# Optimization experiments

Measured on AMD Instinct MI355X. Metric: run time of the kernel, lower is better.

Reference implementation:

```python
import jax, jax.numpy as jnp
import numpy as np

D, H, O, NEXP, NA = 128, 256, 128, 8, 5  # na = max(1, int(8*0.7)) = 5
T = float(np.e)  # gate temperature
N_TOKENS = 131072


def ternary_quantize(w):
    # per-expert-matrix threshold: alpha = mean(|W|) over each [out,in] matrix
    alpha = jnp.mean(jnp.abs(w), axis=(-2, -1), keepdims=True)
    return jnp.sign(w) * (jnp.abs(w) > 0.5 * alpha).astype(w.dtype)


def setup_inputs() -> dict:
    key = jax.random.key(0)
    ks = jax.random.split(key, 7)
    x = jax.random.normal(ks[0], (N_TOKENS, D), dtype=jnp.float32)
    # expert params stacked over expert dim e (nn.Linear layout: [out, in])
    w1 = jax.random.normal(ks[1], (NEXP, H, D), dtype=jnp.float32) * 0.05
    b1 = jax.random.normal(ks[2], (NEXP, H), dtype=jnp.float32) * 0.05
    w2 = jax.random.normal(ks[3], (NEXP, O, H), dtype=jnp.float32) * 0.05
    b2 = jax.random.normal(ks[4], (NEXP, O), dtype=jnp.float32) * 0.05
    wg = jax.random.normal(ks[5], (NEXP, D), dtype=jnp.float32) * 0.05
    bg = jax.random.normal(ks[6], (NEXP,), dtype=jnp.float32) * 0.05
    return {"x": x, "w1": w1, "b1": b1, "w2": w2, "b2": b2, "wg": wg, "bg": bg}


def reference(x, w1, b1, w2, b2, wg, bg):
    # Ternary-quantize expert weights on the fly (TW.forward); dropout in eval mode (identity).
    w1q = ternary_quantize(w1)
    w2q = ternary_quantize(w2)
    # all-expert dense MLP: x [t,d] -> hidden [t,e,h] -> eo [t,e,o]
    hid = jax.nn.relu(jnp.einsum('td,ehd->teh', x, w1q) + b1[None, :, :])
    eo = jnp.einsum('teh,eoh->teo', hid, w2q) + b2[None, :, :]
    # BG gate: tempered softmax, top-k mask, renormalize
    p = jax.nn.softmax((x @ wg.T + bg) / T, axis=-1)          # [t,e]
    _, idx = jax.lax.top_k(p, NA)                             # [t,na]
    m = jnp.sum(jax.nn.one_hot(idx, NEXP, dtype=p.dtype), axis=-2)  # [t,e] 0/1 mask
    w = p * m
    w = w / (jnp.sum(w, axis=-1, keepdims=True) + 1e-8)
    return jnp.einsum('te,teo->to', w, eo)
```

## Files before the change

kernel.cpp:

```cpp
#include <hip/hip_runtime.h>
#include <hip/hip_bf16.h>

typedef unsigned int u32;
typedef unsigned short u16;
using f32x4  = __attribute__((ext_vector_type(4))) float;
using f32x16 = __attribute__((ext_vector_type(16))) float;
using u32x4  = __attribute__((ext_vector_type(4))) u32;
using s16x8  = __attribute__((ext_vector_type(8))) short;

#define DEV static __device__ __forceinline__

DEV u32 pk2(float a, float b) {
  u16 lo = __builtin_bit_cast(u16, __float2bfloat16(a));
  u16 hi = __builtin_bit_cast(u16, __float2bfloat16(b));
  return (u32)lo | ((u32)hi << 16);
}

DEV f32x16 MFMA32(u32x4 a, u32x4 b, f32x16 c) {
  return __builtin_amdgcn_mfma_f32_32x32x16_bf16(
      __builtin_bit_cast(s16x8, a), __builtin_bit_cast(s16x8, b), c, 0, 0, 0);
}

DEV void pl32swap(u32& a, u32& b) {
  asm volatile("v_permlane32_swap_b32 %0, %1" : "+v"(a), "+v"(b));
}

typedef const __attribute__((address_space(1))) u32 gu32;
typedef __attribute__((address_space(3))) u32 lu32;

DEV void load_lds16(const void* g, void* l) {
  __builtin_amdgcn_global_load_lds((gu32*)g, (lu32*)l, 16, 0, 0);
}

__global__ void qalpha(const float* __restrict__ w1, const float* __restrict__ w2,
                       float* __restrict__ alphas) {
  int b = blockIdx.x;
  const float* src = (b < 8 ? w1 : w2) + (size_t)(b & 7) * 32768;
  int tid = threadIdx.x;
  float s = 0.f;
  for (int i = tid; i < 32768; i += 256) s += fabsf(src[i]);
  #pragma unroll
  for (int off = 32; off >= 1; off >>= 1) s += __shfl_down(s, off, 64);
  __shared__ float ws4[4];
  if ((tid & 63) == 0) ws4[tid >> 6] = s;
  __syncthreads();
  if (tid == 0) alphas[b] = (ws4[0] + ws4[1] + ws4[2] + ws4[3]) * (1.f / 32768.f);
}

DEV u16 tq1(float v, float thr) {
  return (fabsf(v) > thr) ? (v > 0.f ? (u16)0x3F80 : (u16)0xBF80) : (u16)0;
}
DEV u32 tq2(float a, float b, float thr) {
  return (u32)tq1(a, thr) | ((u32)tq1(b, thr) << 16);
}

__global__ void qimg(const float* __restrict__ w1, const float* __restrict__ w2,
                     const float* __restrict__ alphas, char* __restrict__ img) {
  int gid = blockIdx.x * 256 + threadIdx.x;
  int l = gid & 63;
  int col = l & 31, hi = l >> 5;
  const float* src;
  float thr;
  char* dst;
  if (gid < 32768) {
    int ks = (gid >> 6) & 7;
    int n  = gid >> 9;
    int e  = n >> 3, ht = n & 7;
    int h  = ht * 32 + col;
    int k0 = ks * 16 + hi * 8;
    src = w1 + (size_t)e * 32768 + h * 128 + k0;
    thr = 0.5f * alphas[e];
    dst = img + (size_t)n * 16384 + ks * 1024 + l * 16;
  } else {
    int id = gid - 32768;
    int sl = (id >> 6) & 7;
    int n  = id >> 9;
    int e  = n >> 3, c = n & 7;
    int ks2 = sl >> 2, ot = sl & 3;
    int o  = ot * 32 + col;
    int k0 = c * 32 + ks2 * 16 + hi * 8;
    src = w2 + (size_t)e * 32768 + o * 256 + k0;
    thr = 0.5f * alphas[8 + e];
    dst = img + (size_t)n * 16384 + 8192 + sl * 1024 + l * 16;
  }
  float4 v0 = *(const float4*)src;
  float4 v1 = *(const float4*)(src + 4);
  u32 q0 = tq2(v0.x, v0.y, thr), q1 = tq2(v0.z, v0.w, thr);
  u32 q2 = tq2(v1.x, v1.y, thr), q3 = tq2(v1.z, v1.w, thr);
  *(uint4*)dst = make_uint4(q0, q1, q2, q3);
}

#define B1_OFF 65536
#define G_OFF  73728
#define SMEM_BYTES 81920

__global__ __launch_bounds__(256, 2) void moe_main(
    const float* __restrict__ x, const float* __restrict__ b1g,
    const float* __restrict__ b2g, const float* __restrict__ wg,
    const float* __restrict__ bg, const char* __restrict__ img,
    float* __restrict__ out) {
  extern __shared__ char smem[];
  float* s_b1 = (float*)(smem + B1_OFF);
  float* s_g  = (float*)(smem + G_OFF);
  const int tid = threadIdx.x;
  const int w = tid >> 6, l = tid & 63;
  const int col = l & 31, hi = l >> 5;
  const int tokw = blockIdx.x * 256 + w * 64;
  const u32 loff = (u32)(l * 16);

  auto stage_pair = [&](int p) {
    const char* src = img + (size_t)p * 32768 + w * 8192 + loff;
    char* dst = smem + (p & 1) * 32768 + w * 8192;
    #pragma unroll
    for (int i = 0; i < 8; ++i)
      load_lds16(src + i * 1024, dst + i * 1024);
  };

  stage_pair(0);

  {
    const float4* s = (const float4*)b1g;
    float4* d = (float4*)s_b1;
    d[tid] = s[tid];
    d[tid + 256] = s[tid + 256];
  }

  u32x4 xf[2][8];
  #pragma unroll
  for (int tt = 0; tt < 2; ++tt) {
    #pragma unroll
    for (int ks = 0; ks < 8; ++ks) {
      const float* xp = x + (size_t)(tokw + tt * 32 + col) * 128 + ks * 16 + hi * 8;
      float4 v0 = *(const float4*)xp;
      float4 v1 = *(const float4*)(xp + 4);
      xf[tt][ks] = (u32x4){pk2(v0.x, v0.y), pk2(v0.z, v0.w),
                           pk2(v1.x, v1.y), pk2(v1.z, v1.w)};
    }
  }

  {
    int t = blockIdx.x * 256 + tid;
    const float4* xr = (const float4*)(x + (size_t)t * 128);
    const float4* wr = (const float4*)wg;
    float lg[8];
    #pragma unroll
    for (int e = 0; e < 8; ++e) lg[e] = bg[e];
    for (int i = 0; i < 32; ++i) {
      float4 xv = xr[i];
      #pragma unroll
      for (int e = 0; e < 8; ++e) {
        float4 wv = wr[e * 32 + i];
        lg[e] += xv.x * wv.x + xv.y * wv.y + xv.z * wv.z + xv.w * wv.w;
      }
    }
    const float invT = 0.36787944117144233f;
    #pragma unroll
    for (int e = 0; e < 8; ++e) lg[e] *= invT;
    float mx = lg[0];
    #pragma unroll
    for (int e = 1; e < 8; ++e) mx = fmaxf(mx, lg[e]);
    float p[8], den = 0.f;
    #pragma unroll
    for (int e = 0; e < 8; ++e) { p[e] = __expf(lg[e] - mx); den += p[e]; }
    float inv = 1.f / den;
    #pragma unroll
    for (int e = 0; e < 8; ++e) p[e] *= inv;
    float gsel[8], wsum = 0.f;
    #pragma unroll
    for (int e = 0; e < 8; ++e) {
      int rank = 0;
      #pragma unroll
      for (int e2 = 0; e2 < 8; ++e2)
        rank += (p[e2] > p[e]) || (p[e2] == p[e] && e2 < e);
      gsel[e] = (rank < 5) ? p[e] : 0.f;
      wsum += gsel[e];
    }
    float r = 1.f / (wsum + 1e-8f);
    #pragma unroll
    for (int e = 0; e < 8; ++e) s_g[e * 256 + tid] = gsel[e] * r;
  }
  __syncthreads();

  f32x16 acc2[4][2];
  {
    u32x4 gf[2];
    #pragma unroll
    for (int tt = 0; tt < 2; ++tt) {
      u32x4 v = (u32x4){0u, 0u, 0u, 0u};
      if (hi == 0) {
        int t = w * 64 + tt * 32 + col;
        v = (u32x4){pk2(s_g[0 * 256 + t], s_g[1 * 256 + t]),
                    pk2(s_g[2 * 256 + t], s_g[3 * 256 + t]),
                    pk2(s_g[4 * 256 + t], s_g[5 * 256 + t]),
                    pk2(s_g[6 * 256 + t], s_g[7 * 256 + t])};
      }
      gf[tt] = v;
    }
    #pragma unroll
    for (int ot = 0; ot < 4; ++ot) {
      u32x4 af = (u32x4){0u, 0u, 0u, 0u};
      if (hi == 0) {
        int o = ot * 32 + col;
        af = (u32x4){pk2(b2g[0 * 128 + o], b2g[1 * 128 + o]),
                     pk2(b2g[2 * 128 + o], b2g[3 * 128 + o]),
                     pk2(b2g[4 * 128 + o], b2g[5 * 128 + o]),
                     pk2(b2g[6 * 128 + o], b2g[7 * 128 + o])};
      }
      f32x16 z{};
      #pragma unroll
      for (int tt = 0; tt < 2; ++tt) acc2[ot][tt] = MFMA32(af, gf[tt], z);
    }
  }

  auto chunk = [&](const char* cb, int e, int ht, float g0, float g1) {
    f32x16 a1_0{}, a1_1{};
    __builtin_amdgcn_s_setprio(1);
    #pragma unroll
    for (int ks = 0; ks < 8; ++ks) {
      u32x4 f = *(const u32x4*)(cb + ks * 1024 + loff);
      a1_0 = MFMA32(f, xf[0][ks], a1_0);
      a1_1 = MFMA32(f, xf[1][ks], a1_1);
    }
    __builtin_amdgcn_s_setprio(0);

    const float* b1b = s_b1 + e * 256 + ht * 32 + hi * 4;
    u32x4 hf[2][2];
    #pragma unroll
    for (int tt = 0; tt < 2; ++tt) {
      const f32x16& a1 = tt ? a1_1 : a1_0;
      const float g = tt ? g1 : g0;
      u32 u[8];
      #pragma unroll
      for (int rg = 0; rg < 4; ++rg) {
        f32x4 bb = *(const f32x4*)(b1b + rg * 8);
        float h0 = fmaxf(a1[rg * 4 + 0] + bb.x, 0.f) * g;
        float h1 = fmaxf(a1[rg * 4 + 1] + bb.y, 0.f) * g;
        float h2 = fmaxf(a1[rg * 4 + 2] + bb.z, 0.f) * g;
        float h3 = fmaxf(a1[rg * 4 + 3] + bb.w, 0.f) * g;
        u[rg * 2 + 0] = pk2(h0, h1);
        u[rg * 2 + 1] = pk2(h2, h3);
      }
      pl32swap(u[0], u[2]);
      pl32swap(u[1], u[3]);
      pl32swap(u[4], u[6]);
      pl32swap(u[5], u[7]);
      hf[0][tt] = (u32x4){u[0], u[1], u[2], u[3]};
      hf[1][tt] = (u32x4){u[4], u[5], u[6], u[7]};
    }

    __builtin_amdgcn_s_setprio(1);
    #pragma unroll
    for (int ks2 = 0; ks2 < 2; ++ks2) {
      #pragma unroll
      for (int ot = 0; ot < 4; ++ot) {
        u32x4 af = *(const u32x4*)(cb + 8192 + (ks2 * 4 + ot) * 1024 + loff);
        acc2[ot][0] = MFMA32(af, hf[ks2][0], acc2[ot][0]);
        acc2[ot][1] = MFMA32(af, hf[ks2][1], acc2[ot][1]);
      }
    }
    __builtin_amdgcn_s_setprio(0);
  };

  #pragma unroll 1
  for (int q = 0; q < 32; ++q) {
    asm volatile("s_waitcnt vmcnt(0)" ::: "memory");
    __builtin_amdgcn_s_barrier();
    __builtin_amdgcn_sched_barrier(0);
    if (q < 31) stage_pair(q + 1);

    const int e = q >> 2, ht0 = (q & 3) * 2;
    const float g0 = s_g[e * 256 + w * 64 + col];
    const float g1 = s_g[e * 256 + w * 64 + 32 + col];
    const char* buf = smem + (q & 1) * 32768;
    chunk(buf, e, ht0, g0, g1);
    __builtin_amdgcn_sched_barrier(0);
    chunk(buf + 16384, e, ht0 + 1, g0, g1);
  }

  #pragma unroll
  for (int ot = 0; ot < 4; ++ot) {
    #pragma unroll
    for (int tt = 0; tt < 2; ++tt) {
      const f32x16& a = acc2[ot][tt];
      float* op = out + (size_t)(tokw + tt * 32 + col) * 128 + ot * 32 + hi * 4;
      #pragma unroll
      for (int rg = 0; rg < 4; ++rg)
        *(f32x4*)(op + rg * 8) =
            (f32x4){a[rg * 4 + 0], a[rg * 4 + 1], a[rg * 4 + 2], a[rg * 4 + 3]};
    }
  }
}

extern "C" void kernel_launch(void* const* d_in, const int* in_sizes, int n_in,
                              void* d_out, int out_size, void* d_ws, size_t ws_size,
                              hipStream_t stream) {
  const float* x  = (const float*)d_in[0];
  const float* w1 = (const float*)d_in[1];
  const float* b1 = (const float*)d_in[2];
  const float* w2 = (const float*)d_in[3];
  const float* b2 = (const float*)d_in[4];
  const float* wg = (const float*)d_in[5];
  const float* bg = (const float*)d_in[6];
  float* out = (float*)d_out;

  if (ws_size < 1048640) return;
  char* ws = (char*)d_ws;
  char* img = ws;
  float* alphas = (float*)(ws + 1048576);

  int ntok = in_sizes[0] / 128;
  int nblk = ntok / 256;

  qalpha<<<16, 256, 0, stream>>>(w1, w2, alphas);
  qimg<<<256, 256, 0, stream>>>(w1, w2, alphas, img);

  hipFuncSetAttribute(reinterpret_cast<const void*>(moe_main),
                      hipFuncAttributeMaxDynamicSharedMemorySize, SMEM_BYTES);
  moe_main<<<nblk, 256, SMEM_BYTES, stream>>>(x, b1, b2, wg, bg, img, out);
}
```

Before: 181.2 us.

## Sort tokens by top-k expert mask and skip unselected experts per block

The gate (softmax plus top-5 selection) moves out of the main kernel into a pre-pass, fused with the weight-quantization kernel. That pre-pass writes per-token gate weights and an 8-bit expert mask and builds a histogram of masks. A scan and scatter then produce a permutation that groups tokens with the same mask. The main kernel reads x through this permutation, ORs the masks within its block, and loops only over the experts in that union, skipping matmuls whose gate weight is zero. The cost is two extra small launches, gathered row loads and scattered output stores, and a loop trip count that varies per block.

```diff
diff --git a/kernel.cpp b/kernel.cpp
--- a/kernel.cpp
+++ b/kernel.cpp
@@ -33,10 +33,11 @@
 }
 
 __global__ void qalpha(const float* __restrict__ w1, const float* __restrict__ w2,
-                       float* __restrict__ alphas) {
+                       float* __restrict__ alphas, u32* __restrict__ hist) {
   int b = blockIdx.x;
+  int tid = threadIdx.x;
+  if (b == 0) hist[tid] = 0;
   const float* src = (b < 8 ? w1 : w2) + (size_t)(b & 7) * 32768;
-  int tid = threadIdx.x;
   float s = 0.f;
   for (int i = tid; i < 32768; i += 256) s += fabsf(src[i]);
   #pragma unroll
@@ -54,40 +55,127 @@
   return (u32)tq1(a, thr) | ((u32)tq1(b, thr) << 16);
 }
 
-__global__ void qimg(const float* __restrict__ w1, const float* __restrict__ w2,
-                     const float* __restrict__ alphas, char* __restrict__ img) {
-  int gid = blockIdx.x * 256 + threadIdx.x;
-  int l = gid & 63;
-  int col = l & 31, hi = l >> 5;
-  const float* src;
-  float thr;
-  char* dst;
-  if (gid < 32768) {
-    int ks = (gid >> 6) & 7;
-    int n  = gid >> 9;
-    int e  = n >> 3, ht = n & 7;
-    int h  = ht * 32 + col;
-    int k0 = ks * 16 + hi * 8;
-    src = w1 + (size_t)e * 32768 + h * 128 + k0;
-    thr = 0.5f * alphas[e];
-    dst = img + (size_t)n * 16384 + ks * 1024 + l * 16;
-  } else {
-    int id = gid - 32768;
-    int sl = (id >> 6) & 7;
-    int n  = id >> 9;
-    int e  = n >> 3, c = n & 7;
-    int ks2 = sl >> 2, ot = sl & 3;
-    int o  = ot * 32 + col;
-    int k0 = c * 32 + ks2 * 16 + hi * 8;
-    src = w2 + (size_t)e * 32768 + o * 256 + k0;
-    thr = 0.5f * alphas[8 + e];
-    dst = img + (size_t)n * 16384 + 8192 + sl * 1024 + l * 16;
-  }
-  float4 v0 = *(const float4*)src;
-  float4 v1 = *(const float4*)(src + 4);
-  u32 q0 = tq2(v0.x, v0.y, thr), q1 = tq2(v0.z, v0.w, thr);
-  u32 q2 = tq2(v1.x, v1.y, thr), q3 = tq2(v1.z, v1.w, thr);
-  *(uint4*)dst = make_uint4(q0, q1, q2, q3);
+__global__ void qimg_gate(const float* __restrict__ w1, const float* __restrict__ w2,
+                          const float* __restrict__ alphas, char* __restrict__ img,
+                          const float* __restrict__ x, const float* __restrict__ wg,
+                          const float* __restrict__ bg, float* __restrict__ gw,
+                          u32* __restrict__ maskA, u32* __restrict__ hist) {
+  const int tid = threadIdx.x;
+  if (blockIdx.x < 256) {
+    int gid = blockIdx.x * 256 + tid;
+    int l = gid & 63;
+    int col = l & 31, hi = l >> 5;
+    const float* src;
+    float thr;
+    char* dst;
+    if (gid < 32768) {
+      int ks = (gid >> 6) & 7;
+      int n  = gid >> 9;
+      int e  = n >> 3, ht = n & 7;
+      int h  = ht * 32 + col;
+      int k0 = ks * 16 + hi * 8;
+      src = w1 + (size_t)e * 32768 + h * 128 + k0;
+      thr = 0.5f * alphas[e];
+      dst = img + (size_t)n * 16384 + ks * 1024 + l * 16;
+    } else {
+      int id = gid - 32768;
+      int sl = (id >> 6) & 7;
+      int n  = id >> 9;
+      int e  = n >> 3, c = n & 7;
+      int ks2 = sl >> 2, ot = sl & 3;
+      int o  = ot * 32 + col;
+      int k0 = c * 32 + ks2 * 16 + hi * 8;
+      src = w2 + (size_t)e * 32768 + o * 256 + k0;
+      thr = 0.5f * alphas[8 + e];
+      dst = img + (size_t)n * 16384 + 8192 + sl * 1024 + l * 16;
+    }
+    float4 v0 = *(const float4*)src;
+    float4 v1 = *(const float4*)(src + 4);
+    *(uint4*)dst = make_uint4(tq2(v0.x, v0.y, thr), tq2(v0.z, v0.w, thr),
+                              tq2(v1.x, v1.y, thr), tq2(v1.z, v1.w, thr));
+    return;
+  }
+  __shared__ u32 lh[256];
+  lh[tid] = 0;
+  int t = (blockIdx.x - 256) * 256 + tid;
+  const float4* xr = (const float4*)(x + (size_t)t * 128);
+  const float4* wr = (const float4*)wg;
+  float lg[8];
+  #pragma unroll
+  for (int e = 0; e < 8; ++e) lg[e] = bg[e];
+  for (int i = 0; i < 32; ++i) {
+    float4 xv = xr[i];
+    #pragma unroll
+    for (int e = 0; e < 8; ++e) {
+      float4 wv = wr[e * 32 + i];
+      lg[e] += xv.x * wv.x + xv.y * wv.y + xv.z * wv.z + xv.w * wv.w;
+    }
+  }
+  const float invT = 0.36787944117144233f;
+  #pragma unroll
+  for (int e = 0; e < 8; ++e) lg[e] *= invT;
+  float mx = lg[0];
+  #pragma unroll
+  for (int e = 1; e < 8; ++e) mx = fmaxf(mx, lg[e]);
+  float p[8], den = 0.f;
+  #pragma unroll
+  for (int e = 0; e < 8; ++e) { p[e] = __expf(lg[e] - mx); den += p[e]; }
+  float inv = 1.f / den;
+  #pragma unroll
+  for (int e = 0; e < 8; ++e) p[e] *= inv;
+  float gsel[8], wsum = 0.f;
+  u32 m = 0;
+  #pragma unroll
+  for (int e = 0; e < 8; ++e) {
+    int rank = 0;
+    #pragma unroll
+    for (int e2 = 0; e2 < 8; ++e2)
+      rank += (p[e2] > p[e]) || (p[e2] == p[e] && e2 < e);
+    bool sel = rank < 5;
+    if (sel) m |= 1u << e;
+    gsel[e] = sel ? p[e] : 0.f;
+    wsum += gsel[e];
+  }
+  float r = 1.f / (wsum + 1e-8f);
+  float* gwp = gw + (size_t)t * 8;
+  *(f32x4*)gwp       = (f32x4){gsel[0] * r, gsel[1] * r, gsel[2] * r, gsel[3] * r};
+  *(f32x4*)(gwp + 4) = (f32x4){gsel[4] * r, gsel[5] * r, gsel[6] * r, gsel[7] * r};
+  maskA[t] = m;
+  __syncthreads();
+  atomicAdd(&lh[m], 1u);
+  __syncthreads();
+  if (lh[tid]) atomicAdd(&hist[tid], lh[tid]);
+}
+
+__global__ void kscan(const u32* __restrict__ hist, u32* __restrict__ cur) {
+  __shared__ u32 s[256];
+  int t = threadIdx.x;
+  u32 own = hist[t];
+  s[t] = own;
+  __syncthreads();
+  #pragma unroll
+  for (int o = 1; o < 256; o <<= 1) {
+    u32 v = (t >= o) ? s[t - o] : 0u;
+    __syncthreads();
+    s[t] += v;
+    __syncthreads();
+  }
+  cur[t] = s[t] - own;
+}
+
+__global__ void kscatter(const u32* __restrict__ maskA, u32* __restrict__ cur,
+                         u32* __restrict__ perm) {
+  __shared__ u32 lh[256], lb[256];
+  const int tid = threadIdx.x;
+  int t = blockIdx.x * 256 + tid;
+  u32 m = maskA[t];
+  lh[tid] = 0;
+  __syncthreads();
+  u32 r = atomicAdd(&lh[m], 1u);
+  __syncthreads();
+  if (lh[tid]) lb[tid] = atomicAdd(&cur[tid], lh[tid]);
+  __syncthreads();
+  perm[lb[m] + r] = t;
 }
 
 #define B1_OFF 65536
@@ -96,29 +184,55 @@
 
 __global__ __launch_bounds__(256, 2) void moe_main(
     const float* __restrict__ x, const float* __restrict__ b1g,
-    const float* __restrict__ b2g, const float* __restrict__ wg,
-    const float* __restrict__ bg, const char* __restrict__ img,
-    float* __restrict__ out) {
+    const float* __restrict__ b2g, const char* __restrict__ img,
+    const u32* __restrict__ perm, const u32* __restrict__ maskA,
+    const float* __restrict__ gw, float* __restrict__ out) {
   extern __shared__ char smem[];
   float* s_b1 = (float*)(smem + B1_OFF);
   float* s_g  = (float*)(smem + G_OFF);
+  u32*   s_u  = (u32*)(smem + G_OFF);
   const int tid = threadIdx.x;
   const int w = tid >> 6, l = tid & 63;
   const int col = l & 31, hi = l >> 5;
-  const int tokw = blockIdx.x * 256 + w * 64;
+  const int base = blockIdx.x * 256;
   const u32 loff = (u32)(l * 16);
 
-  auto stage_pair = [&](int p) {
-    const char* src = img + (size_t)p * 32768 + w * 8192 + loff;
-    char* dst = smem + (p & 1) * 32768 + w * 8192;
+  const u32 ptg = perm[base + tid];
+  const u32 pt0 = perm[base + w * 64 + col];
+  const u32 pt1 = perm[base + w * 64 + 32 + col];
+  s_u[tid] = maskA[ptg];
+  __syncthreads();
+  #pragma unroll
+  for (int st = 128; st >= 1; st >>= 1) {
+    if (tid < st) s_u[tid] |= s_u[tid + st];
+    __syncthreads();
+  }
+  const u32 bmask = s_u[0];
+  __syncthreads();
+
+  u32 elist = 0;
+  int cnt = 0;
+  #pragma unroll
+  for (int e = 0; e < 8; ++e)
+    if ((bmask >> e) & 1) { elist |= (u32)e << (4 * cnt); ++cnt; }
+
+  auto stage_pair = [&](int P, int slot) {
+    const char* src = img + (size_t)P * 32768 + w * 8192 + loff;
+    char* dst = smem + slot * 32768 + w * 8192;
     #pragma unroll
     for (int i = 0; i < 8; ++i)
       load_lds16(src + i * 1024, dst + i * 1024);
   };
 
-  stage_pair(0);
+  stage_pair((elist & 7) * 4, 0);
 
   {
+    f32x4 gA = *(const f32x4*)(gw + (size_t)ptg * 8);
+    f32x4 gB = *(const f32x4*)(gw + (size_t)ptg * 8 + 4);
+    s_g[0 * 256 + tid] = gA.x; s_g[1 * 256 + tid] = gA.y;
+    s_g[2 * 256 + tid] = gA.z; s_g[3 * 256 + tid] = gA.w;
+    s_g[4 * 256 + tid] = gB.x; s_g[5 * 256 + tid] = gB.y;
+    s_g[6 * 256 + tid] = gB.z; s_g[7 * 256 + tid] = gB.w;
     const float4* s = (const float4*)b1g;
     float4* d = (float4*)s_b1;
     d[tid] = s[tid];
@@ -128,56 +242,15 @@
   u32x4 xf[2][8];
   #pragma unroll
   for (int tt = 0; tt < 2; ++tt) {
+    const u32 pt = tt ? pt1 : pt0;
     #pragma unroll
     for (int ks = 0; ks < 8; ++ks) {
-      const float* xp = x + (size_t)(tokw + tt * 32 + col) * 128 + ks * 16 + hi * 8;
+      const float* xp = x + (size_t)pt * 128 + ks * 16 + hi * 8;
       float4 v0 = *(const float4*)xp;
       float4 v1 = *(const float4*)(xp + 4);
       xf[tt][ks] = (u32x4){pk2(v0.x, v0.y), pk2(v0.z, v0.w),
                            pk2(v1.x, v1.y), pk2(v1.z, v1.w)};
     }
-  }
-
-  {
-    int t = blockIdx.x * 256 + tid;
-    const float4* xr = (const float4*)(x + (size_t)t * 128);
-    const float4* wr = (const float4*)wg;
-    float lg[8];
-    #pragma unroll
-    for (int e = 0; e < 8; ++e) lg[e] = bg[e];
-    for (int i = 0; i < 32; ++i) {
-      float4 xv = xr[i];
-      #pragma unroll
-      for (int e = 0; e < 8; ++e) {
-        float4 wv = wr[e * 32 + i];
-        lg[e] += xv.x * wv.x + xv.y * wv.y + xv.z * wv.z + xv.w * wv.w;
-      }
-    }
-    const float invT = 0.36787944117144233f;
-    #pragma unroll
-    for (int e = 0; e < 8; ++e) lg[e] *= invT;
-    float mx = lg[0];
-    #pragma unroll
-    for (int e = 1; e < 8; ++e) mx = fmaxf(mx, lg[e]);
-    float p[8], den = 0.f;
-    #pragma unroll
-    for (int e = 0; e < 8; ++e) { p[e] = __expf(lg[e] - mx); den += p[e]; }
-    float inv = 1.f / den;
-    #pragma unroll
-    for (int e = 0; e < 8; ++e) p[e] *= inv;
-    float gsel[8], wsum = 0.f;
-    #pragma unroll
-    for (int e = 0; e < 8; ++e) {
-      int rank = 0;
-      #pragma unroll
-      for (int e2 = 0; e2 < 8; ++e2)
-        rank += (p[e2] > p[e]) || (p[e2] == p[e] && e2 < e);
-      gsel[e] = (rank < 5) ? p[e] : 0.f;
-      wsum += gsel[e];
-    }
-    float r = 1.f / (wsum + 1e-8f);
-    #pragma unroll
-    for (int e = 0; e < 8; ++e) s_g[e * 256 + tid] = gsel[e] * r;
   }
   __syncthreads();
 
@@ -261,20 +334,25 @@
     __builtin_amdgcn_s_setprio(0);
   };
 
+  const int iters = cnt * 4;
   #pragma unroll 1
-  for (int q = 0; q < 32; ++q) {
+  for (int i = 0; i < iters; ++i) {
     asm volatile("s_waitcnt vmcnt(0)" ::: "memory");
     __builtin_amdgcn_s_barrier();
     __builtin_amdgcn_sched_barrier(0);
-    if (q < 31) stage_pair(q + 1);
-
-    const int e = q >> 2, ht0 = (q & 3) * 2;
-    const float g0 = s_g[e * 256 + w * 64 + col];
-    const float g1 = s_g[e * 256 + w * 64 + 32 + col];
-    const char* buf = smem + (q & 1) * 32768;
-    chunk(buf, e, ht0, g0, g1);
+    if (i + 1 < iters) {
+      const int j = i + 1;
+      const int ej = (elist >> (4 * (j >> 2))) & 7;
+      stage_pair(ej * 4 + (j & 3), j & 1);
+    }
+    const int ei = (elist >> (4 * (i >> 2))) & 7;
+    const int ht0 = (i & 3) * 2;
+    const float g0 = s_g[ei * 256 + w * 64 + col];
+    const float g1 = s_g[ei * 256 + w * 64 + 32 + col];
+    const char* buf = smem + (i & 1) * 32768;
+    chunk(buf, ei, ht0, g0, g1);
     __builtin_amdgcn_sched_barrier(0);
-    chunk(buf + 16384, e, ht0 + 1, g0, g1);
+    chunk(buf + 16384, ei, ht0 + 1, g0, g1);
   }
 
   #pragma unroll
@@ -282,7 +360,7 @@
     #pragma unroll
     for (int tt = 0; tt < 2; ++tt) {
       const f32x16& a = acc2[ot][tt];
-      float* op = out + (size_t)(tokw + tt * 32 + col) * 128 + ot * 32 + hi * 4;
+      float* op = out + (size_t)(tt ? pt1 : pt0) * 128 + ot * 32 + hi * 4;
       #pragma unroll
       for (int rg = 0; rg < 4; ++rg)
         *(f32x4*)(op + rg * 8) =
@@ -303,18 +381,26 @@
   const float* bg = (const float*)d_in[6];
   float* out = (float*)d_out;
 
-  if (ws_size < 1048640) return;
   char* ws = (char*)d_ws;
-  char* img = ws;
+  char*  img    = ws;
   float* alphas = (float*)(ws + 1048576);
+  u32*   hist   = (u32*)(ws + 1048640);
+  u32*   cur    = (u32*)(ws + 1049664);
+  u32*   maskA  = (u32*)(ws + 1050688);
+  u32*   perm   = (u32*)(ws + 1574976);
+  float* gw     = (float*)(ws + 2099264);
+  if (ws_size < 6293568) return;
 
   int ntok = in_sizes[0] / 128;
   int nblk = ntok / 256;
 
-  qalpha<<<16, 256, 0, stream>>>(w1, w2, alphas);
-  qimg<<<256, 256, 0, stream>>>(w1, w2, alphas, img);
+  qalpha<<<16, 256, 0, stream>>>(w1, w2, alphas, hist);
+  qimg_gate<<<256 + nblk, 256, 0, stream>>>(w1, w2, alphas, img, x, wg, bg,
+                                            gw, maskA, hist);
+  kscan<<<1, 256, 0, stream>>>(hist, cur);
+  kscatter<<<nblk, 256, 0, stream>>>(maskA, cur, perm);
 
   hipFuncSetAttribute(reinterpret_cast<const void*>(moe_main),
                       hipFuncAttributeMaxDynamicSharedMemorySize, SMEM_BYTES);
-  moe_main<<<nblk, 256, SMEM_BYTES, stream>>>(x, b1, b2, wg, bg, img, out);
-}
+  moe_main<<<nblk, 256, SMEM_BYTES, stream>>>(x, b1, b2, img, perm, maskA, gw, out);
+}
```

Result: slower. 208.7 us (+15.1%).
